# Kernel tuning notes

Hardware: AMD Instinct MI355X
Metric: run time of the kernel (lower is better)

Reference implementation:

```python
import jax, jax.numpy as jnp
import numpy as np

N = 20000   # nodes
E = 160000  # edges
C = 512     # input_size / channels
D = 16      # edge_size
H = 256     # hidden_size
EPS = 1e-5  # BatchNorm eps (eval mode, init running stats: mean=0, var=1)


def setup_inputs() -> dict:
    key = jax.random.key(0)
    ks = jax.random.split(key, 24)
    w = lambda k, shape: (jax.random.normal(k, shape, jnp.float32) * 0.02)
    inp = {
        "x": jax.random.normal(ks[0], (N, C), jnp.float32),
        "edge_index": jax.random.randint(ks[1], (2, E), 0, N, jnp.int32),
        "edge_attr": jax.random.normal(ks[2], (E, D), jnp.float32),
        "goal_feat": jax.random.normal(ks[3], (N, C), jnp.float32),
        # CGConv 1
        "Wf1": w(ks[4], (2 * C + D, C)), "bf1": jnp.zeros((C,), jnp.float32),
        "Ws1": w(ks[5], (2 * C + D, C)), "bs1": jnp.zeros((C,), jnp.float32),
        "g1": jnp.ones((C,), jnp.float32), "be1": jnp.zeros((C,), jnp.float32),
        # CGConv 2
        "Wf2": w(ks[6], (2 * C + D, C)), "bf2": jnp.zeros((C,), jnp.float32),
        "Ws2": w(ks[7], (2 * C + D, C)), "bs2": jnp.zeros((C,), jnp.float32),
        "g2": jnp.ones((C,), jnp.float32), "be2": jnp.zeros((C,), jnp.float32),
        # GCNConv 3, 4
        "W3": w(ks[8], (C, H)), "b3": jnp.zeros((H,), jnp.float32),
        "W4": w(ks[9], (H, H)), "b4": jnp.zeros((H,), jnp.float32),
        # distance MLP: Lin(H+C -> C), ReLU, Lin(C -> 1)
        "Wd1": w(ks[10], (H + C, C)), "bd1": jnp.zeros((C,), jnp.float32),
        "Wd2": w(ks[11], (C, 1)), "bd2": jnp.zeros((1,), jnp.float32),
    }
    return inp


def cg_conv(x, src, dst, edge_attr, Wf, bf, Ws, bs, gamma, beta):
    # PyG CGConv: z = x_i || x_j || e;  m = sigmoid(lin_f(z)) * softplus(lin_s(z))
    # aggr='add' at targets, BatchNorm (eval, init stats), residual.
    z = jnp.concatenate([x[dst], x[src], edge_attr], axis=-1)  # [E, 2C+D]
    m = jax.nn.sigmoid(z @ Wf + bf) * jax.nn.softplus(z @ Ws + bs)  # [E, C]
    agg = jax.ops.segment_sum(m, dst, num_segments=N)  # [N, C]
    agg = agg * (gamma / jnp.sqrt(1.0 + EPS)) + beta   # BN eval (mean=0, var=1)
    return agg + x


def gcn_conv(x, src, dst, W, b):
    # PyG GCNConv with add_self_loops=True, normalize=True
    h = x @ W  # [N, out]
    loop = jnp.arange(N, dtype=src.dtype)
    s = jnp.concatenate([src, loop])
    d = jnp.concatenate([dst, loop])
    deg = jax.ops.segment_sum(jnp.ones_like(d, jnp.float32), d, num_segments=N)
    dinv = jnp.where(deg > 0, jax.lax.rsqrt(jnp.maximum(deg, 1.0)), 0.0)
    norm = dinv[s] * dinv[d]  # [E+N]
    out = jax.ops.segment_sum(norm[:, None] * h[s], d, num_segments=N)
    return out + b


def reference(x, edge_index, edge_attr, goal_feat,
              Wf1, bf1, Ws1, bs1, g1, be1,
              Wf2, bf2, Ws2, bs2, g2, be2,
              W3, b3, W4, b4, Wd1, bd1, Wd2, bd2):
    src = edge_index[0]  # x_j (source)
    dst = edge_index[1]  # x_i (target)
    h = jax.nn.relu(cg_conv(x, src, dst, edge_attr, Wf1, bf1, Ws1, bs1, g1, be1))
    h = jax.nn.relu(cg_conv(h, src, dst, edge_attr, Wf2, bf2, Ws2, bs2, g2, be2))
    h = jax.nn.relu(gcn_conv(h, src, dst, W3, b3))
    h = jax.nn.relu(gcn_conv(h, src, dst, W4, b4))
    z = jnp.concatenate([h, goal_feat], axis=1)  # [N, H+C]
    pred_dist = jax.nn.relu(z @ Wd1 + bd1) @ Wd2 + bd2  # [N, 1]
    return pred_dist, h
```

## Files before the change

kernel.cpp:

```cpp
#include <hip/hip_runtime.h>
#include <stdint.h>

#define NNODES 20000
#define NEDGES 160000
#define NPAD   20096

typedef float f32x4 __attribute__((ext_vector_type(4)));
typedef float f32x2 __attribute__((ext_vector_type(2)));
typedef short s16x8 __attribute__((ext_vector_type(8)));
typedef unsigned int u32x4 __attribute__((ext_vector_type(4)));
typedef _Float16 h16x2 __attribute__((ext_vector_type(2)));

#define L2E 1.44269504088896340736f
#define LN2 0.6931471805599453f

__device__ __forceinline__ float b2f(unsigned short b) {
    unsigned int u = ((unsigned int)b) << 16;
    return __builtin_bit_cast(float, u);
}
__device__ __forceinline__ unsigned short f2b(float f) {
    unsigned int u = __builtin_bit_cast(unsigned int, f);
    unsigned int r = (u + 0x7FFFu + ((u >> 16) & 1u)) >> 16;
    return (unsigned short)r;
}
__device__ __forceinline__ f32x2 unpack2(unsigned int u) {
    f32x2 r;
    r.x = __builtin_bit_cast(float, u << 16);
    r.y = __builtin_bit_cast(float, u & 0xFFFF0000u);
    return r;
}
__device__ __forceinline__ unsigned int packh2(float a, float b) {
    h16x2 h = { (_Float16)a, (_Float16)b };
    return __builtin_bit_cast(unsigned int, h);
}
__device__ __forceinline__ float dot2h(unsigned int a, unsigned int b, float c) {
#if __has_builtin(__builtin_amdgcn_fdot2)
    return __builtin_amdgcn_fdot2(__builtin_bit_cast(h16x2, a),
                                  __builtin_bit_cast(h16x2, b), c, false);
#else
    float d;
    asm("v_dot2_f32_f16 %0, %1, %2, %3" : "=v"(d) : "v"(a), "v"(b), "v"(c));
    return d;
#endif
}
__device__ __forceinline__ float exp2f_fast(float x) {
#if __has_builtin(__builtin_amdgcn_exp2f)
    return __builtin_amdgcn_exp2f(x);
#else
    return __builtin_exp2f(x);
#endif
}
__device__ __forceinline__ float log2f_fast(float x) {
#if __has_builtin(__builtin_amdgcn_logf)
    return __builtin_amdgcn_logf(x);
#else
    return __builtin_log2f(x);
#endif
}

__global__ __launch_bounds__(256) void gemm_bt_kernel(
    const unsigned short* __restrict__ A,
    const unsigned short* __restrict__ BT,
    float* __restrict__ Cf,
    unsigned short* __restrict__ Cb,
    int M, int N, int K,
    const float* __restrict__ bias)
{
    __shared__ unsigned short As[128 * 64];
    __shared__ unsigned short Bs[128 * 64];
    const int tid  = threadIdx.x;
    const int wid  = tid >> 6;
    const int lane = tid & 63;
    const int bm = blockIdx.x * 128;
    const int bn = blockIdx.y * 128;
    const int wm = (wid & 1) * 64;
    const int wn = (wid >> 1) * 64;

    f32x4 acc[4][4];
#pragma unroll
    for (int i = 0; i < 4; i++)
#pragma unroll
        for (int j = 0; j < 4; j++) acc[i][j] = {0.f, 0.f, 0.f, 0.f};

    for (int k0 = 0; k0 < K; k0 += 64) {
#pragma unroll
        for (int r = 0; r < 4; r++) {
            int flat = r * 256 + tid;
            int row  = flat >> 3;
            int part = flat & 7;
            int pg   = part ^ (row & 7);
            const unsigned short* ga = A  + (size_t)(bm + row) * K + k0 + pg * 8;
            const unsigned short* gb = BT + (size_t)(bn + row) * K + k0 + pg * 8;
            __builtin_amdgcn_global_load_lds(
                (const __attribute__((address_space(1))) unsigned int*)ga,
                (__attribute__((address_space(3))) unsigned int*)&As[flat * 8], 16, 0, 0);
            __builtin_amdgcn_global_load_lds(
                (const __attribute__((address_space(1))) unsigned int*)gb,
                (__attribute__((address_space(3))) unsigned int*)&Bs[flat * 8], 16, 0, 0);
        }
        __syncthreads();

        const int kq8 = lane >> 4;
        const int rl  = lane & 15;
#pragma unroll
        for (int kk = 0; kk < 2; kk++) {
            s16x8 af[4], bfr[4];
#pragma unroll
            for (int mi = 0; mi < 4; mi++) {
                int row = wm + mi * 16 + rl;
                int slot = (kk * 4 + kq8) ^ (row & 7);
                af[mi] = *(const s16x8*)&As[row * 64 + slot * 8];
            }
#pragma unroll
            for (int ni = 0; ni < 4; ni++) {
                int row = wn + ni * 16 + rl;
                int slot = (kk * 4 + kq8) ^ (row & 7);
                bfr[ni] = *(const s16x8*)&Bs[row * 64 + slot * 8];
            }
#pragma unroll
            for (int mi = 0; mi < 4; mi++)
#pragma unroll
                for (int ni = 0; ni < 4; ni++)
                    acc[mi][ni] = __builtin_amdgcn_mfma_f32_16x16x32_bf16(
                        af[mi], bfr[ni], acc[mi][ni], 0, 0, 0);
        }
        __syncthreads();
    }

    const int cl = lane & 15;
    const int rq = (lane >> 4) * 4;
#pragma unroll
    for (int mi = 0; mi < 4; mi++)
#pragma unroll
        for (int ni = 0; ni < 4; ni++)
#pragma unroll
            for (int r = 0; r < 4; r++) {
                int row = bm + wm + mi * 16 + rq + r;
                int col = bn + wn + ni * 16 + cl;
                float v = acc[mi][ni][r];
                if (Cb) {
                    if (bias) v = fmaxf(v + bias[col], 0.f);
                    Cb[(size_t)row * N + col] = f2b(v);
                } else {
                    Cf[(size_t)row * N + col] = v;
                }
            }
}

__global__ void count_kernel(const int* __restrict__ ei, int* __restrict__ counts) {
    int e = blockIdx.x * blockDim.x + threadIdx.x;
    if (e < NEDGES) atomicAdd(&counts[ei[NEDGES + e]], 1);
}

__global__ __launch_bounds__(1024) void scan_kernel(const int* __restrict__ counts,
                                                    int* __restrict__ row_ptr)
{
    __shared__ int sdata[1024];
    const int t = threadIdx.x;
    int vals[20];
    const int base = t * 20;
    int lsum = 0;
#pragma unroll
    for (int j = 0; j < 20; j++) {
        int idx = base + j;
        int v = (idx < NNODES) ? counts[idx] : 0;
        vals[j] = v; lsum += v;
    }
    sdata[t] = lsum;
    __syncthreads();
    for (int off = 1; off < 1024; off <<= 1) {
        int v = (t >= off) ? sdata[t - off] : 0;
        __syncthreads();
        sdata[t] += v;
        __syncthreads();
    }
    int run = sdata[t] - lsum;
#pragma unroll
    for (int j = 0; j < 20; j++) {
        int idx = base + j;
        if (idx < NNODES) row_ptr[idx] = run;
        run += vals[j];
    }
    if (t == 1023) row_ptr[NNODES] = sdata[1023];
}

__global__ void fill_kernel(const int* __restrict__ ei,
                            const int* __restrict__ row_ptr,
                            int* __restrict__ cursor,
                            int* __restrict__ csr_src,
                            int* __restrict__ csr_eid)
{
    int e = blockIdx.x * blockDim.x + threadIdx.x;
    if (e >= NEDGES) return;
    int dst = ei[NEDGES + e];
    int p = row_ptr[dst] + atomicAdd(&cursor[dst], 1);
    csr_src[p] = ei[e];
    csr_eid[p] = e;
}

__global__ void dinv_kernel(const int* __restrict__ row_ptr, float* __restrict__ dinv) {
    int i = blockIdx.x * blockDim.x + threadIdx.x;
    if (i < NNODES) {
        int deg = row_ptr[i + 1] - row_ptr[i] + 1;
        dinv[i] = rsqrtf((float)deg);
    }
}

__global__ void pad_copy_kernel(const float* __restrict__ src,
                                unsigned short* __restrict__ dst,
                                int valid_rows, int cols, long total)
{
    long idx = (long)blockIdx.x * blockDim.x + threadIdx.x;
    if (idx >= total) return;
    int n = (int)(idx / cols);
    dst[idx] = (n < valid_rows) ? f2b(src[idx]) : (unsigned short)0;
}

__global__ void pack_cgw_kernel(const float* __restrict__ Wf,
                                const float* __restrict__ Ws,
                                unsigned short* __restrict__ out)
{
    int idx = blockIdx.x * blockDim.x + threadIdx.x;
    if (idx >= 2048 * 512) return;
    int j = idx >> 9;
    int k = idx & 511;
    int half = (j >= 1024);
    int jj = j & 1023;
    int c  = (jj >> 2) * 2 + (jj & 1);
    int fs = (jj >> 1) & 1;
    const float* W = fs ? Ws : Wf;
    float v = W[(size_t)(half ? 512 + k : k) * 512 + c] * L2E;
    out[idx] = f2b(v);
}

__global__ void pack_t_kernel(const float* __restrict__ W,
                              unsigned short* __restrict__ WT,
                              int K, int Nout)
{
    long idx = (long)blockIdx.x * blockDim.x + threadIdx.x;
    if (idx >= (long)K * Nout) return;
    int j = (int)(idx / K);
    int k = (int)(idx % K);
    WT[idx] = f2b(W[(size_t)k * Nout + j]);
}

__global__ void pack_we_kernel(const float* __restrict__ Wf,
                               const float* __restrict__ Ws,
                               unsigned int* __restrict__ out)
{
    int idx = blockIdx.x * blockDim.x + threadIdx.x;
    if (idx >= 8192) return;
    int tid = idx >> 5;
    int r   = idx & 31;
    int k   = r >> 2;
    int q   = r & 3;
    const float* W = (q >> 1) ? Ws : Wf;
    int c = tid * 2 + (q & 1);
    float v0 = W[(size_t)(1024 + 2 * k) * 512 + c] * L2E;
    float v1 = W[(size_t)(1024 + 2 * k + 1) * 512 + c] * L2E;
    out[idx] = packh2(v0, v1);
}

__global__ void pack_ea_kernel(const int* __restrict__ csr_eid,
                               const float* __restrict__ ea,
                               unsigned int* __restrict__ out)
{
    int idx = blockIdx.x * blockDim.x + threadIdx.x;
    if (idx >= NEDGES * 8) return;
    int i = idx >> 3;
    int j = idx & 7;
    int eid = csr_eid[i];
    out[idx] = packh2(ea[(size_t)eid * 16 + 2 * j], ea[(size_t)eid * 16 + 2 * j + 1]);
}

#define CG_NPB 4

#define CG_LOADE(q_, a0_, a1_, jj) do {                                        \
    int sx_ = __builtin_amdgcn_readlane(sxv, (jj));                            \
    q_  = *(const uint2*)(P + (size_t)sx_ * 2048 + 1024 + c0 * 2);             \
    a0_ = eapk[(size_t)(base + (jj)) * 2];                                     \
    a1_ = eapk[(size_t)(base + (jj)) * 2 + 1];                                 \
} while (0)

#define CG_COMP(q_, a0_, a1_) do {                                             \
    float f0 = baseF.x, f1 = baseF.y, s0 = baseS.x, s1 = baseS.y;              \
    f0 = dot2h(a0_[0], w0[0], f0); f1 = dot2h(a0_[0], w0[1], f1);              \
    s0 = dot2h(a0_[0], w0[2], s0); s1 = dot2h(a0_[0], w0[3], s1);              \
    f0 = dot2h(a0_[1], w1[0], f0); f1 = dot2h(a0_[1], w1[1], f1);              \
    s0 = dot2h(a0_[1], w1[2], s0); s1 = dot2h(a0_[1], w1[3], s1);              \
    f0 = dot2h(a0_[2], w2[0], f0); f1 = dot2h(a0_[2], w2[1], f1);              \
    s0 = dot2h(a0_[2], w2[2], s0); s1 = dot2h(a0_[2], w2[3], s1);              \
    f0 = dot2h(a0_[3], w3[0], f0); f1 = dot2h(a0_[3], w3[1], f1);              \
    s0 = dot2h(a0_[3], w3[2], s0); s1 = dot2h(a0_[3], w3[3], s1);              \
    f0 = dot2h(a1_[0], w4[0], f0); f1 = dot2h(a1_[0], w4[1], f1);              \
    s0 = dot2h(a1_[0], w4[2], s0); s1 = dot2h(a1_[0], w4[3], s1);              \
    f0 = dot2h(a1_[1], w5[0], f0); f1 = dot2h(a1_[1], w5[1], f1);              \
    s0 = dot2h(a1_[1], w5[2], s0); s1 = dot2h(a1_[1], w5[3], s1);              \
    f0 = dot2h(a1_[2], w6[0], f0); f1 = dot2h(a1_[2], w6[1], f1);              \
    s0 = dot2h(a1_[2], w6[2], s0); s1 = dot2h(a1_[2], w6[3], s1);              \
    f0 = dot2h(a1_[3], w7[0], f0); f1 = dot2h(a1_[3], w7[1], f1);              \
    s0 = dot2h(a1_[3], w7[2], s0); s1 = dot2h(a1_[3], w7[3], s1);              \
    f32x2 pf = unpack2(q_.x);                                                  \
    f32x2 ps = unpack2(q_.y);                                                  \
    f0 += pf.x; f1 += pf.y; s0 += ps.x; s1 += ps.y;                            \
    float sp0 = log2f_fast(1.f + exp2f_fast(s0));                              \
    float sp1 = log2f_fast(1.f + exp2f_fast(s1));                              \
    float sg0 = __builtin_amdgcn_rcpf(1.f + exp2f_fast(-f0));                  \
    float sg1 = __builtin_amdgcn_rcpf(1.f + exp2f_fast(-f1));                  \
    acc.x = fmaf(sp0, sg0, acc.x);                                             \
    acc.y = fmaf(sp1, sg1, acc.y);                                             \
} while (0)

__global__ __launch_bounds__(256, 1) void cg_gather_kernel(
    const unsigned short* __restrict__ P,
    const int* __restrict__ row_ptr,
    const int* __restrict__ csr_src,
    const unsigned int* __restrict__ wE,
    const u32x4* __restrict__ eapk,
    const float* __restrict__ bfv,
    const float* __restrict__ bsv,
    const float* __restrict__ g,
    const float* __restrict__ be,
    const float* __restrict__ xresf,
    const unsigned short* __restrict__ xresb,
    unsigned short* __restrict__ hout)
{
    const int tid  = threadIdx.x;
    const int lane = tid & 63;
    const int c0  = tid * 2;
    const int nbase = blockIdx.x * CG_NPB;

    const unsigned int* wp = wE + (size_t)tid * 32;
    u32x4 w0, w1, w2, w3, w4, w5, w6, w7;
    asm volatile(
        "global_load_dwordx4 %0, %8, off\n\t"
        "global_load_dwordx4 %1, %8, off offset:16\n\t"
        "global_load_dwordx4 %2, %8, off offset:32\n\t"
        "global_load_dwordx4 %3, %8, off offset:48\n\t"
        "global_load_dwordx4 %4, %8, off offset:64\n\t"
        "global_load_dwordx4 %5, %8, off offset:80\n\t"
        "global_load_dwordx4 %6, %8, off offset:96\n\t"
        "global_load_dwordx4 %7, %8, off offset:112\n\t"
        "s_waitcnt vmcnt(0)"
        : "=&v"(w0), "=&v"(w1), "=&v"(w2), "=&v"(w3),
          "=&v"(w4), "=&v"(w5), "=&v"(w6), "=&v"(w7)
        : "v"(wp));
    __builtin_amdgcn_sched_barrier(0);

    const f32x2 bfx = *(const f32x2*)&bfv[c0] * L2E;
    const f32x2 bsx = *(const f32x2*)&bsv[c0] * L2E;
    const f32x2 gv  = *(const f32x2*)&g[c0];
    const f32x2 bev = *(const f32x2*)&be[c0];
    const float rsl = rsqrtf(1.f + 1e-5f) * LN2;

    for (int n = nbase; n < nbase + CG_NPB; n++) {
        if (n >= NNODES) {
            *(unsigned int*)&hout[(size_t)n * 512 + c0] = 0;
            continue;
        }
        const unsigned short* Pd = P + (size_t)n * 2048;
        const uint2 qb = *(const uint2*)(Pd + c0 * 2);
        const f32x2 baseF = unpack2(qb.x) + bfx;
        const f32x2 baseS = unpack2(qb.y) + bsx;

        f32x2 acc = {0.f, 0.f};
        const int i0 = __builtin_amdgcn_readfirstlane(row_ptr[n]);
        const int i1 = __builtin_amdgcn_readfirstlane(row_ptr[n + 1]);

        for (int base = i0; base < i1; base += 64) {
            const int cnt = min(64, i1 - base);
            int idxc = base + lane;
            if (idxc >= NEDGES) idxc = NEDGES - 1;
            const int sxv = csr_src[idxc];

            uint2 qA = {}, qB = {};
            u32x4 aA0 = {}, aA1 = {}, aB0 = {}, aB1 = {};
            CG_LOADE(qA, aA0, aA1, 0);
            if (cnt > 1) CG_LOADE(qB, aB0, aB1, 1);
            int j = 0;
            while (true) {
                CG_COMP(qA, aA0, aA1);
                if (j + 2 < cnt) CG_LOADE(qA, aA0, aA1, j + 2);
                if (++j >= cnt) break;
                CG_COMP(qB, aB0, aB1);
                if (j + 2 < cnt) CG_LOADE(qB, aB0, aB1, j + 2);
                if (++j >= cnt) break;
            }
        }

        f32x2 res;
        if (xresf) {
            res = *(const f32x2*)&xresf[(size_t)n * 512 + c0];
        } else {
            res = unpack2(*(const unsigned int*)&xresb[(size_t)n * 512 + c0]);
        }
        float v0 = fmaxf(acc.x * (gv.x * rsl) + bev.x + res.x, 0.f);
        float v1 = fmaxf(acc.y * (gv.y * rsl) + bev.y + res.y, 0.f);
        unsigned int packed = (unsigned int)f2b(v0) | ((unsigned int)f2b(v1) << 16);
        *(unsigned int*)&hout[(size_t)n * 512 + c0] = packed;
    }
}

__global__ __launch_bounds__(256) void gcn_gather_kernel(
    const unsigned short* __restrict__ pre,
    const int* __restrict__ row_ptr,
    const int* __restrict__ csr_src,
    const float* __restrict__ dinv,
    const float* __restrict__ b,
    unsigned short* __restrict__ hout,
    float* __restrict__ doutf)
{
    const int tid  = threadIdx.x;
    const int lane = tid & 63;
    const int n = blockIdx.x * 4 + (tid >> 6);
    const int c = lane * 4;
    if (n >= NNODES) {
        if (n < NPAD) { uint2 z = {0u, 0u}; *(uint2*)&hout[(size_t)n * 256 + c] = z; }
        return;
    }
    const float din = dinv[n];
    f32x4 acc = {0.f, 0.f, 0.f, 0.f};
    const int i0 = __builtin_amdgcn_readfirstlane(row_ptr[n]);
    const int i1 = __builtin_amdgcn_readfirstlane(row_ptr[n + 1]);

#define GCN_LD(pv_, jj) do {                                                   \
    int sx_ = __builtin_amdgcn_readlane(sxv, (jj));                            \
    pv_ = *(const uint2*)&pre[(size_t)sx_ * 256 + c];                          \
} while (0)

#define GCN_CP(pv_, jj) do {                                                   \
    float dv_ = __builtin_bit_cast(float, __builtin_amdgcn_readlane(dvb, (jj)));\
    f32x2 p0 = unpack2(pv_.x);                                                 \
    f32x2 p1 = unpack2(pv_.y);                                                 \
    acc.x = fmaf(dv_, p0.x, acc.x);                                            \
    acc.y = fmaf(dv_, p0.y, acc.y);                                            \
    acc.z = fmaf(dv_, p1.x, acc.z);                                            \
    acc.w = fmaf(dv_, p1.y, acc.w);                                            \
} while (0)

    for (int base = i0; base < i1; base += 64) {
        const int cnt = min(64, i1 - base);
        int idxc = base + lane;
        if (idxc >= NEDGES) idxc = NEDGES - 1;
        const int sxv = csr_src[idxc];
        const int dvb = __builtin_bit_cast(int, dinv[sxv]);

        uint2 pvA = {}, pvB = {}, pvC = {};
        GCN_LD(pvA, 0);
        if (cnt > 1) GCN_LD(pvB, 1);
        if (cnt > 2) GCN_LD(pvC, 2);
        int j = 0;
        while (true) {
            GCN_CP(pvA, j);
            if (j + 3 < cnt) GCN_LD(pvA, j + 3);
            if (++j >= cnt) break;
            GCN_CP(pvB, j);
            if (j + 3 < cnt) GCN_LD(pvB, j + 3);
            if (++j >= cnt) break;
            GCN_CP(pvC, j);
            if (j + 3 < cnt) GCN_LD(pvC, j + 3);
            if (++j >= cnt) break;
        }
    }
    uint2 sv = *(const uint2*)&pre[(size_t)n * 256 + c];
    f32x2 s0 = unpack2(sv.x);
    f32x2 s1 = unpack2(sv.y);
    const f32x4 bv = *(const f32x4*)&b[c];
    const float d2 = din * din;
    float v0 = fmaxf(fmaf(acc.x, din, d2 * s0.x) + bv.x, 0.f);
    float v1 = fmaxf(fmaf(acc.y, din, d2 * s0.y) + bv.y, 0.f);
    float v2 = fmaxf(fmaf(acc.z, din, d2 * s1.x) + bv.z, 0.f);
    float v3 = fmaxf(fmaf(acc.w, din, d2 * s1.y) + bv.w, 0.f);
    uint2 o;
    o.x = (unsigned int)f2b(v0) | ((unsigned int)f2b(v1) << 16);
    o.y = (unsigned int)f2b(v2) | ((unsigned int)f2b(v3) << 16);
    *(uint2*)&hout[(size_t)n * 256 + c] = o;
    if (doutf) {
        f32x4 vv = {v0, v1, v2, v3};
        *(f32x4*)&doutf[(size_t)n * 256 + c] = vv;
    }
}

__global__ void build_zc_kernel(const unsigned short* __restrict__ h4,
                                const float* __restrict__ goal,
                                unsigned short* __restrict__ zc)
{
    long idx = (long)blockIdx.x * blockDim.x + threadIdx.x;
    if (idx >= (long)NPAD * 768) return;
    int n = (int)(idx / 768);
    int c = (int)(idx % 768);
    unsigned short v = 0;
    if (n < NNODES)
        v = (c < 256) ? h4[(size_t)n * 256 + c]
                      : f2b(goal[(size_t)n * 512 + (c - 256)]);
    zc[idx] = v;
}

__global__ __launch_bounds__(256) void final_dot_kernel(
    const unsigned short* __restrict__ t,
    const float* __restrict__ Wd2,
    const float* __restrict__ bd2,
    float* __restrict__ pred)
{
    const int lane = threadIdx.x & 63;
    const int wid  = threadIdx.x >> 6;
    float w[8];
#pragma unroll
    for (int i = 0; i < 8; i++) w[i] = Wd2[lane * 8 + i];
    const float bd = bd2[0];
    for (int n = blockIdx.x * 4 + wid; n < NNODES; n += gridDim.x * 4) {
        const unsigned short* tp = t + (size_t)n * 512 + lane * 8;
        float s = 0.f;
#pragma unroll
        for (int i = 0; i < 8; i++) s = fmaf(b2f(tp[i]), w[i], s);
#pragma unroll
        for (int off = 32; off; off >>= 1) s += __shfl_xor(s, off, 64);
        if (lane == 0) pred[n] = s + bd;
    }
}

extern "C" void kernel_launch(void* const* d_in, const int* in_sizes, int n_in,
                              void* d_out, int out_size, void* d_ws, size_t ws_size,
                              hipStream_t stream)
{
    (void)in_sizes; (void)n_in; (void)out_size; (void)ws_size;
    const float* x    = (const float*)d_in[0];
    const int*   ei   = (const int*)d_in[1];
    const float* ea   = (const float*)d_in[2];
    const float* goal = (const float*)d_in[3];
    const float* Wf1  = (const float*)d_in[4];
    const float* bf1  = (const float*)d_in[5];
    const float* Ws1  = (const float*)d_in[6];
    const float* bs1  = (const float*)d_in[7];
    const float* g1   = (const float*)d_in[8];
    const float* be1  = (const float*)d_in[9];
    const float* Wf2  = (const float*)d_in[10];
    const float* bf2  = (const float*)d_in[11];
    const float* Ws2  = (const float*)d_in[12];
    const float* bs2  = (const float*)d_in[13];
    const float* g2   = (const float*)d_in[14];
    const float* be2  = (const float*)d_in[15];
    const float* W3   = (const float*)d_in[16];
    const float* b3   = (const float*)d_in[17];
    const float* W4   = (const float*)d_in[18];
    const float* b4   = (const float*)d_in[19];
    const float* Wd1  = (const float*)d_in[20];
    const float* bd1  = (const float*)d_in[21];
    const float* Wd2  = (const float*)d_in[22];
    const float* bd2  = (const float*)d_in[23];
    float* outp = (float*)d_out;

    char* ws = (char*)d_ws;
    size_t off = 0;
    auto alloc = [&](size_t bytes) -> char* {
        char* p = ws + off;
        off += (bytes + 255) & ~(size_t)255;
        return p;
    };
    unsigned short* P     = (unsigned short*)alloc((size_t)NPAD * 2048 * 2);
    unsigned short* bufA  = (unsigned short*)alloc((size_t)NPAD * 512 * 2);
    unsigned short* bufB  = (unsigned short*)alloc((size_t)NPAD * 512 * 2);
    unsigned short* bufC  = (unsigned short*)alloc((size_t)NPAD * 512 * 2);
    unsigned short* wpack = (unsigned short*)alloc((size_t)2048 * 512 * 2);
    int*            counts  = (int*)alloc((size_t)NNODES * 4);
    int*            row_ptr = (int*)alloc((size_t)(NNODES + 1) * 4);
    int*            csr_src = (int*)alloc((size_t)NEDGES * 4);
    int*            csr_eid = (int*)alloc((size_t)NEDGES * 4);
    float*          dinv    = (float*)alloc((size_t)NNODES * 4);
    unsigned int*   wEbuf   = (unsigned int*)alloc((size_t)8192 * 4);
    unsigned int*   eapk    = (unsigned int*)alloc((size_t)NEDGES * 8 * 4);

    unsigned short* xpad  = bufA;
    unsigned short* h1    = bufB;
    unsigned short* h2    = bufA;
    unsigned short* pre_b = bufB;
    unsigned short* h3    = bufC;
    unsigned short* h4    = bufA;
    unsigned short* zc    = P;
    unsigned short* tb    = P + (size_t)NPAD * 1024;

    const int B = 256;

    hipMemsetAsync(counts, 0, (size_t)NNODES * 4, stream);
    count_kernel<<<(NEDGES + B - 1) / B, B, 0, stream>>>(ei, counts);
    scan_kernel<<<1, 1024, 0, stream>>>(counts, row_ptr);
    hipMemsetAsync(counts, 0, (size_t)NNODES * 4, stream);
    fill_kernel<<<(NEDGES + B - 1) / B, B, 0, stream>>>(ei, row_ptr, counts, csr_src, csr_eid);
    dinv_kernel<<<(NNODES + B - 1) / B, B, 0, stream>>>(row_ptr, dinv);
    pack_ea_kernel<<<(NEDGES * 8 + B - 1) / B, B, 0, stream>>>(csr_eid, ea, eapk);

    {
        long tot = (long)NPAD * 512;
        pad_copy_kernel<<<(unsigned)((tot + B - 1) / B), B, 0, stream>>>(x, xpad, NNODES, 512, tot);
    }

    dim3 gBig(NPAD / 128, 2048 / 128);

    pack_cgw_kernel<<<(2048 * 512 + B - 1) / B, B, 0, stream>>>(Wf1, Ws1, wpack);
    pack_we_kernel<<<(8192 + B - 1) / B, B, 0, stream>>>(Wf1, Ws1, wEbuf);
    gemm_bt_kernel<<<gBig, B, 0, stream>>>(xpad, wpack, nullptr, P, NPAD, 2048, 512, nullptr);
    cg_gather_kernel<<<NPAD / CG_NPB, B, 0, stream>>>(P, row_ptr, csr_src,
                                                      wEbuf, (const u32x4*)eapk,
                                                      bf1, bs1, g1, be1,
                                                      x, nullptr, h1);

    pack_cgw_kernel<<<(2048 * 512 + B - 1) / B, B, 0, stream>>>(Wf2, Ws2, wpack);
    gemm_bt_kernel<<<gBig, B, 0, stream>>>(h1, wpack, nullptr, P, NPAD, 2048, 512, nullptr);
    pack_we_kernel<<<(8192 + B - 1) / B, B, 0, stream>>>(Wf2, Ws2, wEbuf);
    cg_gather_kernel<<<NPAD / CG_NPB, B, 0, stream>>>(P, row_ptr, csr_src,
                                                      wEbuf, (const u32x4*)eapk,
                                                      bf2, bs2, g2, be2,
                                                      nullptr, h1, h2);

    pack_t_kernel<<<(256 * 512 + B - 1) / B, B, 0, stream>>>(W3, wpack, 512, 256);
    gemm_bt_kernel<<<dim3(NPAD / 128, 2), B, 0, stream>>>(h2, wpack, nullptr, pre_b, NPAD, 256, 512, nullptr);
    gcn_gather_kernel<<<NPAD / 4, B, 0, stream>>>(pre_b, row_ptr, csr_src, dinv, b3, h3, (float*)nullptr);

    pack_t_kernel<<<(256 * 256 + B - 1) / B, B, 0, stream>>>(W4, wpack, 256, 256);
    gemm_bt_kernel<<<dim3(NPAD / 128, 2), B, 0, stream>>>(h3, wpack, nullptr, pre_b, NPAD, 256, 256, nullptr);
    gcn_gather_kernel<<<NPAD / 4, B, 0, stream>>>(pre_b, row_ptr, csr_src, dinv, b4, h4, outp + NNODES);

    build_zc_kernel<<<(unsigned)(((long)NPAD * 768 + B - 1) / B), B, 0, stream>>>(h4, goal, zc);
    pack_t_kernel<<<(512 * 768 + B - 1) / B, B, 0, stream>>>(Wd1, wpack, 768, 512);
    gemm_bt_kernel<<<dim3(NPAD / 128, 4), B, 0, stream>>>(zc, wpack, nullptr, tb, NPAD, 512, 768, bd1);
    final_dot_kernel<<<512, B, 0, stream>>>(tb, Wd2, bd2, outp);
}
```

Baseline: 757.4 us.

## Swizzle GEMM workgroups across XCDs and transpose weight packs via shared-memory tiles

The GEMM kernel remaps each workgroup's linear id so that consecutive tiles go to the same XCD, with the N-tile index varying fastest. Workgroups sharing an A row-block then land on one XCD's L2, improving cache reuse. The weight packing kernels now transpose through a padded 64x65 LDS tile, so both the fp32 reads and the bf16 writes are coalesced instead of strided. This adds a shared-memory staging step, and the swizzle assumes round-robin dispatch of workgroups to XCDs.

```diff
diff --git a/kernel.cpp b/kernel.cpp
--- a/kernel.cpp
+++ b/kernel.cpp
@@ -71,8 +71,16 @@
     const int tid  = threadIdx.x;
     const int wid  = tid >> 6;
     const int lane = tid & 63;
-    const int bm = blockIdx.x * 128;
-    const int bn = blockIdx.y * 128;
+
+    const int nwg  = gridDim.x * gridDim.y;
+    const int orig = blockIdx.y * gridDim.x + blockIdx.x;
+    const int q = nwg >> 3, r = nwg & 7;
+    const int xcd = orig & 7;
+    const int idx = orig >> 3;
+    const int swz = (xcd < r ? xcd * (q + 1) : r * (q + 1) + (xcd - r) * q) + idx;
+    const int bm = (swz / gridDim.y) * 128;
+    const int bn = (swz % gridDim.y) * 128;
+
     const int wm = (wid & 1) * 64;
     const int wn = (wid >> 1) * 64;
 
@@ -84,8 +92,8 @@
 
     for (int k0 = 0; k0 < K; k0 += 64) {
 #pragma unroll
-        for (int r = 0; r < 4; r++) {
-            int flat = r * 256 + tid;
+        for (int rr = 0; rr < 4; rr++) {
+            int flat = rr * 256 + tid;
             int row  = flat >> 3;
             int part = flat & 7;
             int pg   = part ^ (row & 7);
@@ -134,10 +142,10 @@
 #pragma unroll
         for (int ni = 0; ni < 4; ni++)
 #pragma unroll
-            for (int r = 0; r < 4; r++) {
-                int row = bm + wm + mi * 16 + rq + r;
+            for (int rr = 0; rr < 4; rr++) {
+                int row = bm + wm + mi * 16 + rq + rr;
                 int col = bn + wn + ni * 16 + cl;
-                float v = acc[mi][ni][r];
+                float v = acc[mi][ni][rr];
                 if (Cb) {
                     if (bias) v = fmaxf(v + bias[col], 0.f);
                     Cb[(size_t)row * N + col] = f2b(v);
@@ -216,32 +224,45 @@
     dst[idx] = (n < valid_rows) ? f2b(src[idx]) : (unsigned short)0;
 }
 
-__global__ void pack_cgw_kernel(const float* __restrict__ Wf,
-                                const float* __restrict__ Ws,
-                                unsigned short* __restrict__ out)
-{
-    int idx = blockIdx.x * blockDim.x + threadIdx.x;
-    if (idx >= 2048 * 512) return;
-    int j = idx >> 9;
-    int k = idx & 511;
-    int half = (j >= 1024);
-    int jj = j & 1023;
-    int c  = (jj >> 2) * 2 + (jj & 1);
-    int fs = (jj >> 1) & 1;
+__global__ __launch_bounds__(256) void pack_cgw_kernel(
+    const float* __restrict__ Wf,
+    const float* __restrict__ Ws,
+    unsigned short* __restrict__ out)
+{
+    __shared__ float tile[64][65];
+    const int tx  = threadIdx.x & 63;
+    const int ty4 = threadIdx.x >> 6;
+    const int c0 = blockIdx.x * 64;
+    const int k0 = blockIdx.y * 64;
+    const int fs   = blockIdx.z & 1;
+    const int half = blockIdx.z >> 1;
     const float* W = fs ? Ws : Wf;
-    float v = W[(size_t)(half ? 512 + k : k) * 512 + c] * L2E;
-    out[idx] = f2b(v);
-}
-
-__global__ void pack_t_kernel(const float* __restrict__ W,
-                              unsigned short* __restrict__ WT,
-                              int K, int Nout)
-{
-    long idx = (long)blockIdx.x * blockDim.x + threadIdx.x;
-    if (idx >= (long)K * Nout) return;
-    int j = (int)(idx / K);
-    int k = (int)(idx % K);
-    WT[idx] = f2b(W[(size_t)k * Nout + j]);
+    const float* Wb = W + (size_t)(half ? 512 : 0) * 512;
+    for (int rr = ty4; rr < 64; rr += 4)
+        tile[rr][tx] = Wb[(size_t)(k0 + rr) * 512 + (c0 + tx)];
+    __syncthreads();
+    for (int rr = ty4; rr < 64; rr += 4) {
+        int c = c0 + rr;
+        int j = half * 1024 + (c >> 1) * 4 + fs * 2 + (c & 1);
+        out[(size_t)j * 512 + (k0 + tx)] = f2b(tile[tx][rr] * L2E);
+    }
+}
+
+__global__ __launch_bounds__(256) void pack_t_kernel(
+    const float* __restrict__ W,
+    unsigned short* __restrict__ WT,
+    int K, int Nout)
+{
+    __shared__ float tile[64][65];
+    const int tx  = threadIdx.x & 63;
+    const int ty4 = threadIdx.x >> 6;
+    const int j0 = blockIdx.x * 64;
+    const int k0 = blockIdx.y * 64;
+    for (int rr = ty4; rr < 64; rr += 4)
+        tile[rr][tx] = W[(size_t)(k0 + rr) * Nout + (j0 + tx)];
+    __syncthreads();
+    for (int rr = ty4; rr < 64; rr += 4)
+        WT[(size_t)(j0 + rr) * K + (k0 + tx)] = f2b(tile[tx][rr]);
 }
 
 __global__ void pack_we_kernel(const float* __restrict__ Wf,
@@ -596,7 +617,7 @@
 
     dim3 gBig(NPAD / 128, 2048 / 128);
 
-    pack_cgw_kernel<<<(2048 * 512 + B - 1) / B, B, 0, stream>>>(Wf1, Ws1, wpack);
+    pack_cgw_kernel<<<dim3(8, 8, 4), B, 0, stream>>>(Wf1, Ws1, wpack);
     pack_we_kernel<<<(8192 + B - 1) / B, B, 0, stream>>>(Wf1, Ws1, wEbuf);
     gemm_bt_kernel<<<gBig, B, 0, stream>>>(xpad, wpack, nullptr, P, NPAD, 2048, 512, nullptr);
     cg_gather_kernel<<<NPAD / CG_NPB, B, 0, stream>>>(P, row_ptr, csr_src,
@@ -604,7 +625,7 @@
                                                       bf1, bs1, g1, be1,
                                                       x, nullptr, h1);
 
-    pack_cgw_kernel<<<(2048 * 512 + B - 1) / B, B, 0, stream>>>(Wf2, Ws2, wpack);
+    pack_cgw_kernel<<<dim3(8, 8, 4), B, 0, stream>>>(Wf2, Ws2, wpack);
     gemm_bt_kernel<<<gBig, B, 0, stream>>>(h1, wpack, nullptr, P, NPAD, 2048, 512, nullptr);
     pack_we_kernel<<<(8192 + B - 1) / B, B, 0, stream>>>(Wf2, Ws2, wEbuf);
     cg_gather_kernel<<<NPAD / CG_NPB, B, 0, stream>>>(P, row_ptr, csr_src,
@@ -612,16 +633,16 @@
                                                       bf2, bs2, g2, be2,
                                                       nullptr, h1, h2);
 
-    pack_t_kernel<<<(256 * 512 + B - 1) / B, B, 0, stream>>>(W3, wpack, 512, 256);
+    pack_t_kernel<<<dim3(256 / 64, 512 / 64), B, 0, stream>>>(W3, wpack, 512, 256);
     gemm_bt_kernel<<<dim3(NPAD / 128, 2), B, 0, stream>>>(h2, wpack, nullptr, pre_b, NPAD, 256, 512, nullptr);
     gcn_gather_kernel<<<NPAD / 4, B, 0, stream>>>(pre_b, row_ptr, csr_src, dinv, b3, h3, (float*)nullptr);
 
-    pack_t_kernel<<<(256 * 256 + B - 1) / B, B, 0, stream>>>(W4, wpack, 256, 256);
+    pack_t_kernel<<<dim3(256 / 64, 256 / 64), B, 0, stream>>>(W4, wpack, 256, 256);
     gemm_bt_kernel<<<dim3(NPAD / 128, 2), B, 0, stream>>>(h3, wpack, nullptr, pre_b, NPAD, 256, 256, nullptr);
     gcn_gather_kernel<<<NPAD / 4, B, 0, stream>>>(pre_b, row_ptr, csr_src, dinv, b4, h4, outp + NNODES);
 
     build_zc_kernel<<<(unsigned)(((long)NPAD * 768 + B - 1) / B), B, 0, stream>>>(h4, goal, zc);
-    pack_t_kernel<<<(512 * 768 + B - 1) / B, B, 0, stream>>>(Wd1, wpack, 768, 512);
+    pack_t_kernel<<<dim3(512 / 64, 768 / 64), B, 0, stream>>>(Wd1, wpack, 768, 512);
     gemm_bt_kernel<<<dim3(NPAD / 128, 4), B, 0, stream>>>(zc, wpack, nullptr, tb, NPAD, 512, 768, bd1);
     final_dot_kernel<<<512, B, 0, stream>>>(tb, Wd2, bd2, outp);
 }
```

Measured after the change: 751.8 us. Within noise of the previous version (-0.7%).
